# Kernel tuning notes

Measured on AMD Instinct MI355X. Metric: run time of the kernel, lower is better.

Reference implementation:

```python
import jax, jax.numpy as jnp
import numpy as np

N_NODES = 50000
N_EDGES = 800000
K = 8
D_IN = 64
D_OUT = 64


def setup_inputs() -> dict:
    key = jax.random.key(0)
    k1, k2, k3, k4 = jax.random.split(key, 4)
    x = jax.random.normal(k1, (N_NODES, D_IN), dtype=jnp.float32)
    edge_index = jax.random.randint(k2, (2, N_EDGES), 0, N_NODES, dtype=jnp.int64)
    edge_weight = jax.random.uniform(k3, (N_EDGES,), dtype=jnp.float32)
    W = jax.random.normal(k4, (K, D_IN, D_OUT), dtype=jnp.float32) / np.sqrt(D_IN)
    b = jnp.zeros((K, D_OUT), dtype=jnp.float32)
    return {"x": x, "edge_index": edge_index, "edge_weight": edge_weight, "W": W, "b": b}


def reference(x, edge_index, edge_weight, W, b):
    # GCNConv with add_self_loops=True, normalize=True, applied K times in parallel.
    N = x.shape[0]
    loop = jnp.arange(N, dtype=edge_index.dtype)
    src = jnp.concatenate([edge_index[0], loop])           # [E+N] message sources
    dst = jnp.concatenate([edge_index[1], loop])           # [E+N] aggregation targets
    ew = jnp.concatenate([edge_weight, jnp.ones((N,), x.dtype)])  # self-loop weight 1
    # symmetric normalization: deg computed on target index
    deg = jax.ops.segment_sum(ew, dst, num_segments=N)
    dinv = jnp.where(deg > 0, jax.lax.rsqrt(deg), 0.0)
    norm = dinv[src] * ew * dinv[dst]                      # [E+N]
    outs = []
    for k in range(W.shape[0]):                            # fixed small K, structurally distinct params
        h = x @ W[k]                                       # [N, D_OUT]
        agg = jax.ops.segment_sum(norm[:, None] * h[src], dst, num_segments=N)
        outs.append(agg + b[k])
    return jnp.stack(outs, axis=1)                         # [N, K, D_OUT]
```

## Files before the change

kernel.cpp:

```cpp
#include <hip/hip_runtime.h>

#define NN 50000
#define NE 800000

typedef unsigned long long u64;
typedef __attribute__((ext_vector_type(8))) short bf16x8;
typedef __attribute__((ext_vector_type(4))) float f32x4;

#define FXS 33554432.0f
#define FXI (1.0f / 33554432.0f)
#define W16I (1.0f / 65536.0f)

__device__ inline unsigned short bf16rne(float f) {
    unsigned u = __float_as_uint(f);
    unsigned r = (u + 0x7FFFu + ((u >> 16) & 1u)) >> 16;
    return (unsigned short)r;
}

__global__ void k_prep(const float* __restrict__ W, u64* __restrict__ hist,
                       ushort* __restrict__ wswz) {
    int t = blockIdx.x * blockDim.x + threadIdx.x;
    if (t < NN) hist[t] = 0ULL;
    if (t < 4096) {
        int l    = t & 63;
        int tile = (t >> 6) & 3;
        int s    = (t >> 8) & 1;
        int h    = t >> 9;
        int c0   = s * 32 + (l >> 4) * 8;
        int col  = tile * 16 + (l & 15);
        unsigned o[8];
#pragma unroll
        for (int r = 0; r < 8; r++)
            o[r] = bf16rne(W[(h * 64 + c0 + r) * 64 + col]);
        uint4 v = make_uint4(o[0] | (o[1] << 16), o[2] | (o[3] << 16),
                             o[4] | (o[5] << 16), o[6] | (o[7] << 16));
        ((uint4*)wswz)[t] = v;
    }
}

__global__ void k_hist(const int* __restrict__ ei, const float* __restrict__ ew,
                       u64* __restrict__ hist, int* __restrict__ bucket, int E) {
    int t = blockIdx.x * blockDim.x + threadIdx.x;
    int e = t * 4;
    if (e >= E) return;
    int4   s4 = *(const int4*)(ei + e);
    int4   d4 = *(const int4*)(ei + E + e);
    float4 w4 = *(const float4*)(ew + e);
    int   ss[4] = { s4.x, s4.y, s4.z, s4.w };
    int   dd[4] = { d4.x, d4.y, d4.z, d4.w };
    float ww[4] = { w4.x, w4.y, w4.z, w4.w };
    u64 old[4];
#pragma unroll
    for (int j = 0; j < 4; j++) {
        unsigned fx = (unsigned)(ww[j] * FXS + 0.5f);
        old[j] = atomicAdd(&hist[dd[j]], ((u64)1 << 40) | (u64)fx);
    }
#pragma unroll
    for (int j = 0; j < 4; j++) {
        unsigned pos = (unsigned)(old[j] >> 40);
        unsigned w16 = (unsigned)(ww[j] * 65536.0f + 0.5f);
        if (w16 > 65535u) w16 = 65535u;
        if (pos < 64u)
            __builtin_nontemporal_store((int)((w16 << 16) | (unsigned)ss[j]),
                                        &bucket[((unsigned)dd[j] << 6) + pos]);
    }
}

__global__ void k_dinv(const u64* __restrict__ hist, float* __restrict__ dinv, int n) {
    int i = blockIdx.x * blockDim.x + threadIdx.x;
    if (i < n) {
        u64 h = hist[i];
        dinv[i] = rsqrtf(1.0f + (float)(h & 0xFFFFFFFFFFULL) * FXI);
    }
}

__global__ __launch_bounds__(256) void k_fused(const float* __restrict__ x,
                                               const float* __restrict__ dinv,
                                               const u64* __restrict__ hist,
                                               const int4* __restrict__ bucket4,
                                               const ushort* __restrict__ wswz,
                                               const float* __restrict__ bb,
                                               float* __restrict__ out) {
    __shared__ ushort lds[16][72];
    int wave = threadIdx.x >> 6;
    int lane = threadIdx.x & 63;
    int sub  = lane & 15;
    int grp  = lane >> 4;
    int n0   = blockIdx.x * 16;

    for (int nn = 0; nn < 4; nn++) {
        int row  = wave * 4 + nn;
        int node = n0 + row;
        u64 h = hist[node];
        int cnt = (int)(h >> 40);
        if (cnt > 64) cnt = 64;
        float dn = dinv[node];
        f32x4 accA = {0.f, 0.f, 0.f, 0.f};
        f32x4 accB = {0.f, 0.f, 0.f, 0.f};
        const int4* brow = bucket4 + ((size_t)node << 4);
        int4 r0 = brow[0], r1 = brow[1];
        for (int base = 0; base < cnt; base += 8) {
            int4 q0 = r0, q1 = r1;
            if (base + 8 < cnt) {
                int nb = (base >> 2) + 2;
                r0 = brow[nb]; r1 = brow[nb + 1];
            }
            int rec[8] = { q0.x, q0.y, q0.z, q0.w, q1.x, q1.y, q1.z, q1.w };
            bool  vA = (base + grp)     < cnt;
            bool  vB = (base + grp + 4) < cnt;
            int   rA = rec[grp], rB = rec[grp + 4];
            int   sA = vA ? (rA & 0xFFFF) : node;
            int   sB = vB ? (rB & 0xFFFF) : node;
            float wA = vA ? (float)((unsigned)rA >> 16) * W16I : 0.f;
            float wB = vB ? (float)((unsigned)rB >> 16) * W16I : 0.f;
            float nA = (dn * dinv[sA]) * wA;
            float nB = (dn * dinv[sB]) * wB;
            f32x4 gA = *(const f32x4*)(x + ((unsigned)sA << 6) + (sub << 2));
            f32x4 gB = *(const f32x4*)(x + ((unsigned)sB << 6) + (sub << 2));
            accA += nA * gA;
            accB += nB * gB;
        }
        f32x4 tt = accA + accB;
#pragma unroll
        for (int m = 16; m <= 32; m <<= 1) {
            tt.x += __shfl_xor(tt.x, m, 64);
            tt.y += __shfl_xor(tt.y, m, 64);
            tt.z += __shfl_xor(tt.z, m, 64);
            tt.w += __shfl_xor(tt.w, m, 64);
        }
        if (grp == 0) {
            f32x4 xs = *(const f32x4*)(x + ((unsigned)node << 6) + (sub << 2));
            f32x4 res = tt + (dn * dn) * xs;
            ushort4 o = make_ushort4(bf16rne(res.x), bf16rne(res.y),
                                     bf16rne(res.z), bf16rne(res.w));
            *(ushort4*)(&lds[row][sub << 2]) = o;
        }
    }
    __syncthreads();

    int l15  = sub;
    int ksub = grp;
    bf16x8 a0 = *(const bf16x8*)(&lds[l15][ksub * 8]);
    bf16x8 a1 = *(const bf16x8*)(&lds[l15][32 + ksub * 8]);

#pragma unroll
    for (int hh = 0; hh < 2; hh++) {
        int h = wave * 2 + hh;
#pragma unroll
        for (int tl = 0; tl < 4; tl++) {
            bf16x8 b0 = *(const bf16x8*)(wswz + (size_t)(((h * 2 + 0) * 4 + tl) * 64 + lane) * 8);
            bf16x8 b1 = *(const bf16x8*)(wswz + (size_t)(((h * 2 + 1) * 4 + tl) * 64 + lane) * 8);
            f32x4 c = {0.f, 0.f, 0.f, 0.f};
            c = __builtin_amdgcn_mfma_f32_16x16x32_bf16(a0, b0, c, 0, 0, 0);
            c = __builtin_amdgcn_mfma_f32_16x16x32_bf16(a1, b1, c, 0, 0, 0);
            int   dout = h * 64 + tl * 16 + l15;
            float bv   = bb[dout];
#pragma unroll
            for (int r = 0; r < 4; r++) {
                int nd = n0 + (ksub << 2) + r;
                __builtin_nontemporal_store(c[r] + bv, out + (size_t)nd * 512 + dout);
            }
        }
    }
}

extern "C" void kernel_launch(void* const* d_in, const int* in_sizes, int n_in,
                              void* d_out, int out_size, void* d_ws, size_t ws_size,
                              hipStream_t stream) {
    const float* x  = (const float*)d_in[0];
    const int*   ei = (const int*)d_in[1];
    const float* ew = (const float*)d_in[2];
    const float* W  = (const float*)d_in[3];
    const float* b  = (const float*)d_in[4];
    float* out = (float*)d_out;

    char* ws = (char*)d_ws;
    size_t off = 0;
    auto carve = [&](size_t bytes) {
        void* p = ws + off;
        off += (bytes + 255) & ~(size_t)255;
        return p;
    };
    u64*    hist   = (u64*)   carve((size_t)NN * 8);
    int*    bucket = (int*)   carve((size_t)NN * 64 * 4);
    float*  dinv   = (float*) carve((size_t)NN * 4);
    ushort* wswz   = (ushort*)carve((size_t)4096 * 16);
    (void)ws_size; (void)in_sizes; (void)n_in; (void)out_size;

    k_prep<<<(NN + 255) / 256, 256, 0, stream>>>(W, hist, wswz);
    k_hist<<<(NE / 4 + 255) / 256, 256, 0, stream>>>(ei, ew, hist, bucket, NE);
    k_dinv<<<(NN + 255) / 256, 256, 0, stream>>>(hist, dinv, NN);
    k_fused<<<NN / 16, 256, 0, stream>>>(x, dinv, hist, (const int4*)bucket,
                                         wswz, b, out);
}
```

Before: 138.0 us.

## Split fused aggregate+GEMM kernel into separate aggregation and MFMA GEMM kernels

Replaces the single fused kernel, where each wave aggregated four nodes serially into LDS and then ran the MFMA projection, with two kernels. The first handles one node per wave and writes bf16 aggregated features to a workspace buffer. The second reads those features and runs the MFMA GEMM plus bias store. This gives the gather phase more parallel waves and removes the block barrier. The cost is an extra launch and a round trip through global memory of about 6.4 MB.

```diff
diff --git a/kernel.cpp b/kernel.cpp
--- a/kernel.cpp
+++ b/kernel.cpp
@@ -74,74 +74,74 @@
     }
 }
 
-__global__ __launch_bounds__(256) void k_fused(const float* __restrict__ x,
-                                               const float* __restrict__ dinv,
-                                               const u64* __restrict__ hist,
-                                               const int4* __restrict__ bucket4,
-                                               const ushort* __restrict__ wswz,
-                                               const float* __restrict__ bb,
-                                               float* __restrict__ out) {
-    __shared__ ushort lds[16][72];
-    int wave = threadIdx.x >> 6;
+__global__ __launch_bounds__(256) void k_agg(const float* __restrict__ x,
+                                             const float* __restrict__ dinv,
+                                             const u64* __restrict__ hist,
+                                             const int4* __restrict__ bucket4,
+                                             ushort* __restrict__ xaggb, int n) {
+    int node = blockIdx.x * 4 + (threadIdx.x >> 6);
+    if (node >= n) return;
     int lane = threadIdx.x & 63;
     int sub  = lane & 15;
     int grp  = lane >> 4;
+    u64 h = hist[node];
+    int cnt = (int)(h >> 40);
+    if (cnt > 64) cnt = 64;
+    float dn = dinv[node];
+    f32x4 accA = {0.f, 0.f, 0.f, 0.f};
+    f32x4 accB = {0.f, 0.f, 0.f, 0.f};
+    const int4* brow = bucket4 + ((size_t)node << 4);
+    int4 r0 = brow[0], r1 = brow[1];
+    for (int base = 0; base < cnt; base += 8) {
+        int4 q0 = r0, q1 = r1;
+        if (base + 8 < cnt) {
+            int nb = (base >> 2) + 2;
+            r0 = brow[nb]; r1 = brow[nb + 1];
+        }
+        int rec[8] = { q0.x, q0.y, q0.z, q0.w, q1.x, q1.y, q1.z, q1.w };
+        bool  vA = (base + grp)     < cnt;
+        bool  vB = (base + grp + 4) < cnt;
+        int   rA = rec[grp], rB = rec[grp + 4];
+        int   sA = vA ? (rA & 0xFFFF) : node;
+        int   sB = vB ? (rB & 0xFFFF) : node;
+        float wA = vA ? (float)((unsigned)rA >> 16) * W16I : 0.f;
+        float wB = vB ? (float)((unsigned)rB >> 16) * W16I : 0.f;
+        float nA = (dn * dinv[sA]) * wA;
+        float nB = (dn * dinv[sB]) * wB;
+        f32x4 gA = *(const f32x4*)(x + ((unsigned)sA << 6) + (sub << 2));
+        f32x4 gB = *(const f32x4*)(x + ((unsigned)sB << 6) + (sub << 2));
+        accA += nA * gA;
+        accB += nB * gB;
+    }
+    f32x4 tt = accA + accB;
+#pragma unroll
+    for (int m = 16; m <= 32; m <<= 1) {
+        tt.x += __shfl_xor(tt.x, m, 64);
+        tt.y += __shfl_xor(tt.y, m, 64);
+        tt.z += __shfl_xor(tt.z, m, 64);
+        tt.w += __shfl_xor(tt.w, m, 64);
+    }
+    if (grp == 0) {
+        f32x4 xs = *(const f32x4*)(x + ((unsigned)node << 6) + (sub << 2));
+        f32x4 res = tt + (dn * dn) * xs;
+        ushort4 o = make_ushort4(bf16rne(res.x), bf16rne(res.y),
+                                 bf16rne(res.z), bf16rne(res.w));
+        *(ushort4*)(xaggb + ((unsigned)node << 6) + (sub << 2)) = o;
+    }
+}
+
+__global__ __launch_bounds__(256) void k_gemm(const ushort* __restrict__ xaggb,
+                                              const ushort* __restrict__ wswz,
+                                              const float* __restrict__ bb,
+                                              float* __restrict__ out, int n) {
+    int wave = threadIdx.x >> 6;
+    int lane = threadIdx.x & 63;
+    int l15  = lane & 15;
+    int ksub = lane >> 4;
     int n0   = blockIdx.x * 16;
 
-    for (int nn = 0; nn < 4; nn++) {
-        int row  = wave * 4 + nn;
-        int node = n0 + row;
-        u64 h = hist[node];
-        int cnt = (int)(h >> 40);
-        if (cnt > 64) cnt = 64;
-        float dn = dinv[node];
-        f32x4 accA = {0.f, 0.f, 0.f, 0.f};
-        f32x4 accB = {0.f, 0.f, 0.f, 0.f};
-        const int4* brow = bucket4 + ((size_t)node << 4);
-        int4 r0 = brow[0], r1 = brow[1];
-        for (int base = 0; base < cnt; base += 8) {
-            int4 q0 = r0, q1 = r1;
-            if (base + 8 < cnt) {
-                int nb = (base >> 2) + 2;
-                r0 = brow[nb]; r1 = brow[nb + 1];
-            }
-            int rec[8] = { q0.x, q0.y, q0.z, q0.w, q1.x, q1.y, q1.z, q1.w };
-            bool  vA = (base + grp)     < cnt;
-            bool  vB = (base + grp + 4) < cnt;
-            int   rA = rec[grp], rB = rec[grp + 4];
-            int   sA = vA ? (rA & 0xFFFF) : node;
-            int   sB = vB ? (rB & 0xFFFF) : node;
-            float wA = vA ? (float)((unsigned)rA >> 16) * W16I : 0.f;
-            float wB = vB ? (float)((unsigned)rB >> 16) * W16I : 0.f;
-            float nA = (dn * dinv[sA]) * wA;
-            float nB = (dn * dinv[sB]) * wB;
-            f32x4 gA = *(const f32x4*)(x + ((unsigned)sA << 6) + (sub << 2));
-            f32x4 gB = *(const f32x4*)(x + ((unsigned)sB << 6) + (sub << 2));
-            accA += nA * gA;
-            accB += nB * gB;
-        }
-        f32x4 tt = accA + accB;
-#pragma unroll
-        for (int m = 16; m <= 32; m <<= 1) {
-            tt.x += __shfl_xor(tt.x, m, 64);
-            tt.y += __shfl_xor(tt.y, m, 64);
-            tt.z += __shfl_xor(tt.z, m, 64);
-            tt.w += __shfl_xor(tt.w, m, 64);
-        }
-        if (grp == 0) {
-            f32x4 xs = *(const f32x4*)(x + ((unsigned)node << 6) + (sub << 2));
-            f32x4 res = tt + (dn * dn) * xs;
-            ushort4 o = make_ushort4(bf16rne(res.x), bf16rne(res.y),
-                                     bf16rne(res.z), bf16rne(res.w));
-            *(ushort4*)(&lds[row][sub << 2]) = o;
-        }
-    }
-    __syncthreads();
-
-    int l15  = sub;
-    int ksub = grp;
-    bf16x8 a0 = *(const bf16x8*)(&lds[l15][ksub * 8]);
-    bf16x8 a1 = *(const bf16x8*)(&lds[l15][32 + ksub * 8]);
+    bf16x8 a0 = *(const bf16x8*)(xaggb + (size_t)(n0 + l15) * 64 + ksub * 8);
+    bf16x8 a1 = *(const bf16x8*)(xaggb + (size_t)(n0 + l15) * 64 + 32 + ksub * 8);
 
 #pragma unroll
     for (int hh = 0; hh < 2; hh++) {
@@ -184,12 +184,14 @@
     u64*    hist   = (u64*)   carve((size_t)NN * 8);
     int*    bucket = (int*)   carve((size_t)NN * 64 * 4);
     float*  dinv   = (float*) carve((size_t)NN * 4);
+    ushort* xaggb  = (ushort*)carve((size_t)NN * 64 * 2);
     ushort* wswz   = (ushort*)carve((size_t)4096 * 16);
     (void)ws_size; (void)in_sizes; (void)n_in; (void)out_size;
 
     k_prep<<<(NN + 255) / 256, 256, 0, stream>>>(W, hist, wswz);
     k_hist<<<(NE / 4 + 255) / 256, 256, 0, stream>>>(ei, ew, hist, bucket, NE);
     k_dinv<<<(NN + 255) / 256, 256, 0, stream>>>(hist, dinv, NN);
-    k_fused<<<NN / 16, 256, 0, stream>>>(x, dinv, hist, (const int4*)bucket,
-                                         wswz, b, out);
+    k_agg<<<(NN + 3) / 4, 256, 0, stream>>>(x, dinv, hist, (const int4*)bucket,
+                                            xaggb, NN);
+    k_gemm<<<NN / 16, 256, 0, stream>>>(xaggb, wswz, b, out, NN);
 }
```

After: 123.0 us. 10.9% less time.
